# Optimization experiments

Hardware: AMD Instinct MI355X
Metric: run time of the kernel (lower is better)

Reference implementation:

```python
import jax, jax.numpy as jnp
import numpy as np

SHARPNESS = 2


def setup_inputs() -> dict:
    key = jax.random.key(0)
    k1, k2, k3 = jax.random.split(key, 3)
    x = jax.random.normal(k1, (16, 256, 48, 48), dtype=jnp.float32)
    # 1x1 conv == per-pixel linear: weight (out_c, in_c), bias (out_c,)
    W = jax.random.normal(k2, (256, 256), dtype=jnp.float32) * 0.0625
    bias = jax.random.normal(k3, (256,), dtype=jnp.float32) * 0.01
    return {"x": x, "W": W, "bias": bias}


def reference(x, W, bias):
    b, c, h, w = x.shape
    hw = h * w
    # sample-wide L2 norm over the full (c*h*w) vector (faithful to source)
    xn = jnp.linalg.norm(x.reshape(b, -1), axis=1).reshape(b, 1, 1)
    # NOTE: raw reshapes of the (b,c,h,w)-contiguous tensor, NOT transposes
    x1 = x.reshape(b, hw, c) / xn
    x2 = x.reshape(b, c, hw) / xn
    cos = jnp.einsum('bnc,bcm->bnm', x1, x2)          # (b, hw, hw)
    s = jnp.maximum(cos, 0.0) ** SHARPNESS            # relu^sharpness
    # transform block: 1x1 conv
    tr = jnp.einsum('oc,bchw->bohw', W, x) + bias[None, :, None, None]
    tr = tr.reshape(b, hw, c)                         # raw reshape, as in source
    y = jnp.einsum('bnm,bmc->bnc', s, tr)             # (b, hw, c)
    return y.reshape(b, c, h, w)
```

## Files before the change

kernel.cpp:

```cpp
#include <hip/hip_runtime.h>

#define NB 16
#define NC 256
#define HW 2304
#define CHW 589824

typedef __attribute__((ext_vector_type(8))) short bf16x8;
typedef __attribute__((ext_vector_type(16))) float f32x16;

union BF8 { bf16x8 v; unsigned short u[8]; };

__device__ inline unsigned short f2bf(float f) {
  unsigned u = __builtin_bit_cast(unsigned, f);
  u += 0x7fffu + ((u >> 16) & 1u);
  return (unsigned short)(u >> 16);
}

__global__ __launch_bounds__(256) void prep_kernel(const float* __restrict__ x,
                                                   const float* __restrict__ W,
                                                   unsigned short* __restrict__ wp,
                                                   unsigned short* __restrict__ x1p,
                                                   unsigned short* __restrict__ xtp,
                                                   double* __restrict__ partials) {
  __shared__ __align__(16) char smem[33344];
  const int bid = blockIdx.x;
  const int tid = threadIdx.x;

  if (bid < 8) {
    const int rt = bid;
    float* tile = (float*)smem;
    const float4* src = (const float4*)(W + (size_t)rt * 32 * 256);
    #pragma unroll
    for (int it = 0; it < 8; ++it) {
      const int i = tid + 256 * it;
      float4 v = src[i];
      const int fi = 4 * i, row = fi >> 8, col = fi & 255;
      *(float4*)&tile[row * 260 + col] = v;
    }
    __syncthreads();
    const int w = tid >> 6, l = tid & 63, l31 = l & 31, h = l >> 5;
    unsigned short* dst = wp + (size_t)rt * 8192;
    #pragma unroll
    for (int ff = 0; ff < 4; ++ff) {
      const int f = 4 * w + ff;
      BF8 o;
      #pragma unroll
      for (int j = 0; j < 8; ++j)
        o.u[j] = f2bf(tile[l31 * 260 + 16 * f + 8 * h + j]);
      *(bf16x8*)(dst + (((size_t)f) * 64 + l) * 8) = o.v;
    }
  } else if (bid < 8 + 1152) {
    const int e = bid - 8;
    const int nb = e % 72, b = e / 72;
    float* tile = (float*)smem;
    double* red = (double*)(smem + 33280);
    const float4* src = (const float4*)(x + (size_t)b * CHW + nb * 8192);
    double ss = 0.0;
    #pragma unroll
    for (int it = 0; it < 8; ++it) {
      const int i = tid + 256 * it;
      float4 v = src[i];
      const int fi = 4 * i, row = fi >> 8, col = fi & 255;
      *(float4*)&tile[row * 260 + col] = v;
      ss += (double)v.x * v.x + (double)v.y * v.y + (double)v.z * v.z + (double)v.w * v.w;
    }
    #pragma unroll
    for (int off = 32; off > 0; off >>= 1) ss += __shfl_down(ss, off, 64);
    const int w = tid >> 6, l = tid & 63;
    if (l == 0) red[w] = ss;
    __syncthreads();
    if (tid == 0) partials[b * 72 + nb] = red[0] + red[1] + red[2] + red[3];
    const int l31 = l & 31, h = l >> 5;
    unsigned short* dst = x1p + (size_t)b * CHW + (size_t)nb * 8192;
    #pragma unroll
    for (int ff = 0; ff < 4; ++ff) {
      const int f = 4 * w + ff;
      BF8 o;
      #pragma unroll
      for (int j = 0; j < 8; ++j)
        o.u[j] = f2bf(tile[l31 * 260 + 16 * f + 8 * h + j]);
      *(bf16x8*)(dst + (((size_t)f) * 64 + l) * 8) = o.v;
    }
  } else {
    const int e = bid - 1160;
    const int mt = e % 36, kt = (e / 36) % 4, b = e / 144;
    const int m0 = mt * 64, k0 = kt * 64;
    float* tile = (float*)smem;
    const float* xb = x + (size_t)b * CHW;
    #pragma unroll
    for (int it = 0; it < 4; ++it) {
      const int i = tid + 256 * it;
      const int row = i >> 4, c4 = (i & 15) * 4;
      float4 v = *(const float4*)(xb + (size_t)(k0 + row) * HW + m0 + c4);
      *(float4*)&tile[row * 68 + c4] = v;
    }
    __syncthreads();
    const int w = tid >> 6, l = tid & 63, l31 = l & 31, h = l >> 5;
    unsigned short* dst = xtp + (size_t)b * CHW;
    #pragma unroll
    for (int pp = 0; pp < 2; ++pp) {
      const int p = 2 * w + pp, mbl = p >> 2, fl = p & 3;
      BF8 o;
      #pragma unroll
      for (int j = 0; j < 8; ++j)
        o.u[j] = f2bf(tile[(16 * fl + 8 * h + j) * 68 + 32 * mbl + l31]);
      const int mb = 2 * mt + mbl, f = 4 * kt + fl;
      *(bf16x8*)(dst + (((size_t)mb * 16 + f) * 64 + l) * 8) = o.v;
    }
  }
}

__global__ __launch_bounds__(256, 2) void conv_kernel(const unsigned short* __restrict__ wp,
                                                      const float* __restrict__ bias,
                                                      const unsigned short* __restrict__ xtp,
                                                      unsigned short* __restrict__ trflat,
                                                      const double* __restrict__ partials,
                                                      float* __restrict__ inv_xn2) {
  const int bid = blockIdx.x;
  if (bid == 576) {
    const int t = threadIdx.x;
    const int b = t >> 4, i0 = t & 15;
    double v = 0.0;
    for (int i = i0; i < 72; i += 16) v += partials[b * 72 + i];
    v += __shfl_down(v, 8, 64);
    v += __shfl_down(v, 4, 64);
    v += __shfl_down(v, 2, 64);
    v += __shfl_down(v, 1, 64);
    if (i0 == 0) inv_xn2[b] = (float)(1.0 / v);
    return;
  }
  const int xcd = bid & 7, j = bid >> 3;
  const int hi = (j >= 36) ? 1 : 0;
  const int b = xcd + 8 * hi;
  const int ch = j - 36 * hi;
  const int m0 = ch * 64;
  const int tid = threadIdx.x, w = tid >> 6, l = tid & 63, l31 = l & 31, h = l >> 5;
  const unsigned short* xb = xtp + (size_t)b * CHW;
  unsigned short* tb = trflat + (size_t)b * CHW;
  bf16x8 af[2][16];
  #pragma unroll
  for (int rb = 0; rb < 2; ++rb) {
    const int rt = w + 4 * rb;
    #pragma unroll
    for (int f = 0; f < 16; ++f)
      af[rb][f] = *(const bf16x8*)(wp + (((size_t)rt * 16 + f) * 64 + l) * 8);
  }
  f32x16 yacc[2][2];
  #pragma unroll
  for (int rb = 0; rb < 2; ++rb)
    #pragma unroll
    for (int cb = 0; cb < 2; ++cb)
      #pragma unroll
      for (int i = 0; i < 16; ++i) yacc[rb][cb][i] = 0.f;
  #pragma unroll 4
  for (int f = 0; f < 16; ++f) {
    #pragma unroll
    for (int cb = 0; cb < 2; ++cb) {
      const int mb = 2 * ch + cb;
      bf16x8 bv = *(const bf16x8*)(xb + (((size_t)mb * 16 + f) * 64 + l) * 8);
      yacc[0][cb] = __builtin_amdgcn_mfma_f32_32x32x16_bf16(af[0][f], bv, yacc[0][cb], 0, 0, 0);
      yacc[1][cb] = __builtin_amdgcn_mfma_f32_32x32x16_bf16(af[1][f], bv, yacc[1][cb], 0, 0, 0);
    }
  }
  #pragma unroll
  for (int rb = 0; rb < 2; ++rb)
    #pragma unroll
    for (int reg = 0; reg < 16; ++reg) {
      const int row = 32 * (w + 4 * rb) + (reg & 3) + 8 * (reg >> 2) + 4 * h;
      const float bv = bias[row];
      #pragma unroll
      for (int cb = 0; cb < 2; ++cb)
        tb[(size_t)row * HW + m0 + 32 * cb + l31] = f2bf(yacc[rb][cb][reg] + bv);
    }
}

__global__ __launch_bounds__(256) void trpack_kernel(const unsigned short* __restrict__ trflat,
                                                     unsigned short* __restrict__ trp) {
  const int mb = blockIdx.x, half = blockIdx.y, b = blockIdx.z;
  const unsigned short* src = trflat + (size_t)b * CHW + (size_t)mb * 16384 + 128 * half;
  __shared__ unsigned short tile[64 * 136];
  const int tid = threadIdx.x;
  #pragma unroll
  for (int it = 0; it < 4; ++it) {
    const int i = tid + 256 * it;
    const int row = i >> 4, c8 = (i & 15) * 8;
    *(uint4*)&tile[row * 136 + c8] = *(const uint4*)(src + (size_t)row * 256 + c8);
  }
  __syncthreads();
  const int kf = tid >> 6, l = tid & 63, l31 = l & 31, h = l >> 5;
  unsigned short* dst = trp + (size_t)b * CHW + (size_t)mb * 16384;
  #pragma unroll
  for (int cl = 0; cl < 4; ++cl) {
    BF8 o;
    #pragma unroll
    for (int j = 0; j < 8; ++j)
      o.u[j] = tile[(16 * kf + 8 * h + j) * 136 + 32 * cl + l31];
    const int cb8 = 4 * half + cl;
    *(bf16x8*)(dst + (((size_t)cb8 * 4 + kf) * 64 + l) * 8) = o.v;
  }
}

#define CHUNK_BODY(CH, CUR, NXT)                                                                   \
  {                                                                                                \
    const int ch_ = (CH);                                                                          \
    const int pb_ = ch_ & 1;                                                                       \
    f32x16 s0, s1;                                                                                 \
    _Pragma("unroll")                                                                              \
    for (int i = 0; i < 16; ++i) { s0[i] = 0.f; s1[i] = 0.f; }                                     \
    _Pragma("unroll")                                                                              \
    for (int f = 0; f < 16; ++f) {                                                                 \
      bf16x8 a0 = *(const bf16x8*)(Af + f * 512 + lane * 8);                                       \
      bf16x8 a1 = *(const bf16x8*)(Af + (16 + f) * 512 + lane * 8);                                \
      s0 = __builtin_amdgcn_mfma_f32_32x32x16_bf16(a0, CUR[f], s0, 0, 0, 0);                       \
      s1 = __builtin_amdgcn_mfma_f32_32x32x16_bf16(a1, CUR[f], s1, 0, 0, 0);                       \
    }                                                                                              \
    bf16x8 bt0[8], bt1[8];                                                                         \
    _Pragma("unroll")                                                                              \
    for (int kk = 0; kk < 8; ++kk) {                                                               \
      const size_t mb_ = 2 * ch_ + (kk >> 2);                                                      \
      bt0[kk] = *(const bf16x8*)(ttb + mb_ * 16384 + ((size_t)((2 * c) * 4 + (kk & 3))) * 512 + lane * 8);     \
      bt1[kk] = *(const bf16x8*)(ttb + mb_ * 16384 + ((size_t)((2 * c + 1) * 4 + (kk & 3))) * 512 + lane * 8); \
    }                                                                                              \
    _Pragma("unroll")                                                                              \
    for (int reg = 0; reg < 16; ++reg) {                                                           \
      const int rowp = (reg & 3) + 8 * (reg >> 2) + 4 * h;                                         \
      float v0 = fmaxf(s0[reg] * inv2, 0.f); v0 *= v0;                                             \
      float v1 = fmaxf(s1[reg] * inv2, 0.f); v1 *= v1;                                             \
      Pl[pb_][rowp][32 * c + l31] = f2bf(v0);                                                      \
      Pl[pb_][32 + rowp][32 * c + l31] = f2bf(v1);                                                 \
    }                                                                                              \
    const int chn_ = (ch_ < 17) ? ch_ + 1 : 17;                                                    \
    const unsigned short* bpn_ = xtb + (size_t)((4 * chn_ + c) * 16) * 512 + lane * 8;             \
    _Pragma("unroll")                                                                              \
    for (int f = 0; f < 16; ++f) NXT[f] = *(const bf16x8*)(bpn_ + f * 512);                        \
    __syncthreads();                                                                               \
    _Pragma("unroll")                                                                              \
    for (int kk = 0; kk < 8; ++kk) {                                                               \
      bf16x8 pf0 = *(const bf16x8*)&Pl[pb_][l31][16 * kk + 8 * h];                                 \
      bf16x8 pf1 = *(const bf16x8*)&Pl[pb_][32 + l31][16 * kk + 8 * h];                            \
      yacc[0][0] = __builtin_amdgcn_mfma_f32_32x32x16_bf16(pf0, bt0[kk], yacc[0][0], 0, 0, 0);     \
      yacc[1][0] = __builtin_amdgcn_mfma_f32_32x32x16_bf16(pf1, bt0[kk], yacc[1][0], 0, 0, 0);     \
      yacc[0][1] = __builtin_amdgcn_mfma_f32_32x32x16_bf16(pf0, bt1[kk], yacc[0][1], 0, 0, 0);     \
      yacc[1][1] = __builtin_amdgcn_mfma_f32_32x32x16_bf16(pf1, bt1[kk], yacc[1][1], 0, 0, 0);     \
    }                                                                                              \
  }

__global__ __launch_bounds__(256, 2) void fused_kernel(const unsigned short* __restrict__ x1p,
                                                       const unsigned short* __restrict__ xtp,
                                                       const unsigned short* __restrict__ trp,
                                                       const float* __restrict__ inv_xn2,
                                                       float* __restrict__ out) {
  const int bid = blockIdx.x;
  const int xcd = bid & 7, j = bid >> 3;
  const int hi = (j >= 36) ? 1 : 0;
  const int b = xcd + 8 * hi;
  const int nt = j - 36 * hi;
  const unsigned short* x1b = x1p + (size_t)b * CHW + (size_t)nt * 16384;
  const unsigned short* xtb = xtp + (size_t)b * CHW;
  const unsigned short* ttb = trp + (size_t)b * CHW;
  float* ob = out + (size_t)b * CHW;
  const float inv2 = inv_xn2[b];

  const int tid = threadIdx.x;
  const int c = tid >> 6, lane = tid & 63;
  const int l31 = lane & 31, h = lane >> 5;

  __shared__ unsigned short Af[16384];
  __shared__ unsigned short Pl[2][64][136];

  {
    const uint4* gsrc = (const uint4*)x1b;
    uint4* ldst = (uint4*)Af;
    #pragma unroll
    for (int it = 0; it < 8; ++it) ldst[tid + 256 * it] = gsrc[tid + 256 * it];
  }

  bf16x8 bva[16], bvb[16];
  {
    const unsigned short* bp0 = xtb + (size_t)(c * 16) * 512 + lane * 8;
    #pragma unroll
    for (int f = 0; f < 16; ++f) bva[f] = *(const bf16x8*)(bp0 + f * 512);
  }
  __syncthreads();

  f32x16 yacc[2][2];
  #pragma unroll
  for (int nh = 0; nh < 2; ++nh)
    #pragma unroll
    for (int cb = 0; cb < 2; ++cb)
      #pragma unroll
      for (int i = 0; i < 16; ++i) yacc[nh][cb][i] = 0.f;

  for (int ci = 0; ci < 9; ++ci) {
    CHUNK_BODY(2 * ci, bva, bvb)
    CHUNK_BODY(2 * ci + 1, bvb, bva)
  }

  #pragma unroll
  for (int nh = 0; nh < 2; ++nh)
    #pragma unroll
    for (int cb = 0; cb < 2; ++cb) {
      const int col = 64 * c + 32 * cb + l31;
      #pragma unroll
      for (int reg = 0; reg < 16; ++reg) {
        const int rowp = (reg & 3) + 8 * (reg >> 2) + 4 * h;
        ob[(size_t)(64 * nt + 32 * nh + rowp) * NC + col] = yacc[nh][cb][reg];
      }
    }
}

extern "C" void kernel_launch(void* const* d_in, const int* in_sizes, int n_in,
                              void* d_out, int out_size, void* d_ws, size_t ws_size,
                              hipStream_t stream) {
  const float* x    = (const float*)d_in[0];
  const float* W    = (const float*)d_in[1];
  const float* bias = (const float*)d_in[2];
  float* out = (float*)d_out;

  const size_t SZ = (size_t)NB * CHW * sizeof(unsigned short);
  double* partials       = (double*)d_ws;
  float* inv_xn2         = (float*)((char*)d_ws + 16384);
  unsigned short* wp     = (unsigned short*)((char*)d_ws + 32768);
  unsigned short* x1p    = (unsigned short*)((char*)d_ws + 163840);
  unsigned short* xtp    = (unsigned short*)((char*)d_ws + 163840 + SZ);
  unsigned short* trflat = (unsigned short*)((char*)d_ws + 163840 + 2 * SZ);
  unsigned short* trp    = (unsigned short*)((char*)d_ws + 163840 + 3 * SZ);

  prep_kernel<<<3464, 256, 0, stream>>>(x, W, wp, x1p, xtp, partials);
  conv_kernel<<<577, 256, 0, stream>>>(wp, bias, xtp, trflat, partials, inv_xn2);
  trpack_kernel<<<dim3(36, 2, 16), 256, 0, stream>>>(trflat, trp);
  fused_kernel<<<576, 256, 0, stream>>>(x1p, xtp, trp, inv_xn2, out);
}
```

Measured before the change: 249.9 us.

## Fuse 1x1 conv with transform repack via LDS tile, dropping trflat round-trip

Merges the conv and trpack kernels into one. Each block computes a 32-row slab of the transform output for one batch, stages it in a large LDS tile, then writes it straight into the packed MFMA layout that the fused kernel consumes. This removes a kernel launch and the write-then-read of the intermediate flat bf16 tensor. In exchange the grid shrinks from 577 to 129 blocks with one block per CU because of the ~148KB LDS tile, which cuts parallelism, and the repack reads use divide-by-9 index math.

```diff
diff --git a/kernel.cpp b/kernel.cpp
--- a/kernel.cpp
+++ b/kernel.cpp
@@ -110,14 +110,14 @@
   }
 }
 
-__global__ __launch_bounds__(256, 2) void conv_kernel(const unsigned short* __restrict__ wp,
-                                                      const float* __restrict__ bias,
-                                                      const unsigned short* __restrict__ xtp,
-                                                      unsigned short* __restrict__ trflat,
-                                                      const double* __restrict__ partials,
-                                                      float* __restrict__ inv_xn2) {
+__global__ __launch_bounds__(256, 1) void conv2_kernel(const unsigned short* __restrict__ wp,
+                                                       const float* __restrict__ bias,
+                                                       const unsigned short* __restrict__ xtp,
+                                                       unsigned short* __restrict__ trp,
+                                                       const double* __restrict__ partials,
+                                                       float* __restrict__ inv_xn2) {
   const int bid = blockIdx.x;
-  if (bid == 576) {
+  if (bid == 128) {
     const int t = threadIdx.x;
     const int b = t >> 4, i0 = t & 15;
     double v = 0.0;
@@ -129,74 +129,57 @@
     if (i0 == 0) inv_xn2[b] = (float)(1.0 / v);
     return;
   }
-  const int xcd = bid & 7, j = bid >> 3;
-  const int hi = (j >= 36) ? 1 : 0;
-  const int b = xcd + 8 * hi;
-  const int ch = j - 36 * hi;
-  const int m0 = ch * 64;
+  const int xcd = bid & 7, q = bid >> 3;
+  const int b = xcd + 8 * (q & 1);
+  const int rt = q >> 1;
   const int tid = threadIdx.x, w = tid >> 6, l = tid & 63, l31 = l & 31, h = l >> 5;
   const unsigned short* xb = xtp + (size_t)b * CHW;
-  unsigned short* tb = trflat + (size_t)b * CHW;
-  bf16x8 af[2][16];
+
+  __shared__ unsigned short tile[32 * 2312];
+
+  bf16x8 af[16];
   #pragma unroll
-  for (int rb = 0; rb < 2; ++rb) {
-    const int rt = w + 4 * rb;
-    #pragma unroll
-    for (int f = 0; f < 16; ++f)
-      af[rb][f] = *(const bf16x8*)(wp + (((size_t)rt * 16 + f) * 64 + l) * 8);
-  }
-  f32x16 yacc[2][2];
+  for (int f = 0; f < 16; ++f)
+    af[f] = *(const bf16x8*)(wp + (((size_t)rt * 16 + f) * 64 + l) * 8);
+  float bcol[16];
   #pragma unroll
-  for (int rb = 0; rb < 2; ++rb)
-    #pragma unroll
-    for (int cb = 0; cb < 2; ++cb)
-      #pragma unroll
-      for (int i = 0; i < 16; ++i) yacc[rb][cb][i] = 0.f;
-  #pragma unroll 4
-  for (int f = 0; f < 16; ++f) {
-    #pragma unroll
-    for (int cb = 0; cb < 2; ++cb) {
-      const int mb = 2 * ch + cb;
+  for (int reg = 0; reg < 16; ++reg) {
+    const int rowl = (reg & 3) + 8 * (reg >> 2) + 4 * h;
+    bcol[reg] = bias[32 * rt + rowl];
+  }
+
+  for (int i = 0; i < 18; ++i) {
+    const int mb = 18 * w + i;
+    f32x16 acc;
+    #pragma unroll
+    for (int r = 0; r < 16; ++r) acc[r] = 0.f;
+    #pragma unroll
+    for (int f = 0; f < 16; ++f) {
       bf16x8 bv = *(const bf16x8*)(xb + (((size_t)mb * 16 + f) * 64 + l) * 8);
-      yacc[0][cb] = __builtin_amdgcn_mfma_f32_32x32x16_bf16(af[0][f], bv, yacc[0][cb], 0, 0, 0);
-      yacc[1][cb] = __builtin_amdgcn_mfma_f32_32x32x16_bf16(af[1][f], bv, yacc[1][cb], 0, 0, 0);
-    }
-  }
-  #pragma unroll
-  for (int rb = 0; rb < 2; ++rb)
+      acc = __builtin_amdgcn_mfma_f32_32x32x16_bf16(af[f], bv, acc, 0, 0, 0);
+    }
     #pragma unroll
     for (int reg = 0; reg < 16; ++reg) {
-      const int row = 32 * (w + 4 * rb) + (reg & 3) + 8 * (reg >> 2) + 4 * h;
-      const float bv = bias[row];
-      #pragma unroll
-      for (int cb = 0; cb < 2; ++cb)
-        tb[(size_t)row * HW + m0 + 32 * cb + l31] = f2bf(yacc[rb][cb][reg] + bv);
-    }
-}
-
-__global__ __launch_bounds__(256) void trpack_kernel(const unsigned short* __restrict__ trflat,
-                                                     unsigned short* __restrict__ trp) {
-  const int mb = blockIdx.x, half = blockIdx.y, b = blockIdx.z;
-  const unsigned short* src = trflat + (size_t)b * CHW + (size_t)mb * 16384 + 128 * half;
-  __shared__ unsigned short tile[64 * 136];
-  const int tid = threadIdx.x;
-  #pragma unroll
-  for (int it = 0; it < 4; ++it) {
-    const int i = tid + 256 * it;
-    const int row = i >> 4, c8 = (i & 15) * 8;
-    *(uint4*)&tile[row * 136 + c8] = *(const uint4*)(src + (size_t)row * 256 + c8);
+      const int rowl = (reg & 3) + 8 * (reg >> 2) + 4 * h;
+      tile[rowl * 2312 + mb * 32 + l31] = f2bf(acc[reg] + bcol[reg]);
+    }
   }
   __syncthreads();
-  const int kf = tid >> 6, l = tid & 63, l31 = l & 31, h = l >> 5;
-  unsigned short* dst = trp + (size_t)b * CHW + (size_t)mb * 16384;
-  #pragma unroll
-  for (int cl = 0; cl < 4; ++cl) {
+
+  unsigned short* tb = trp + (size_t)b * CHW;
+  for (int si = 0; si < 36; ++si) {
+    const int id = 36 * w + si;
+    const int kfi = id >> 3, cb8 = id & 7;
+    const int mbase = 288 * rt + 16 * kfi;
+    const int mb2 = mbase >> 6, kf = (mbase >> 4) & 3;
     BF8 o;
     #pragma unroll
-    for (int j = 0; j < 8; ++j)
-      o.u[j] = tile[(16 * kf + 8 * h + j) * 136 + 32 * cl + l31];
-    const int cb8 = 4 * half + cl;
-    *(bf16x8*)(dst + (((size_t)cb8 * 4 + kf) * 64 + l) * 8) = o.v;
+    for (int j = 0; j < 8; ++j) {
+      const int m = mbase + 8 * h + j;
+      const int a = m / 9, s = m - 9 * a;
+      o.u[j] = tile[(a - 32 * rt) * 2312 + 256 * s + 32 * cb8 + l31];
+    }
+    *(bf16x8*)(tb + (size_t)mb2 * 16384 + (((size_t)cb8 * 4 + kf) * 64 + l) * 8) = o.v;
   }
 }
 
@@ -323,11 +306,9 @@
   unsigned short* wp     = (unsigned short*)((char*)d_ws + 32768);
   unsigned short* x1p    = (unsigned short*)((char*)d_ws + 163840);
   unsigned short* xtp    = (unsigned short*)((char*)d_ws + 163840 + SZ);
-  unsigned short* trflat = (unsigned short*)((char*)d_ws + 163840 + 2 * SZ);
   unsigned short* trp    = (unsigned short*)((char*)d_ws + 163840 + 3 * SZ);
 
   prep_kernel<<<3464, 256, 0, stream>>>(x, W, wp, x1p, xtp, partials);
-  conv_kernel<<<577, 256, 0, stream>>>(wp, bias, xtp, trflat, partials, inv_xn2);
-  trpack_kernel<<<dim3(36, 2, 16), 256, 0, stream>>>(trflat, trp);
+  conv2_kernel<<<129, 256, 0, stream>>>(wp, bias, xtp, trp, partials, inv_xn2);
   fused_kernel<<<576, 256, 0, stream>>>(x1p, xtp, trp, inv_xn2, out);
 }
```

New measurement: 258.7 us. +3.5%, slower.
